# Optimization experiments

Measured on AMD Instinct MI355X. Metric: run time of the kernel, lower is better.

## Reference

```python
import jax, jax.numpy as jnp
import numpy as np

BATCH, SEQ, IN, HID, OUT = 128, 1024, 256, 512, 256


def setup_inputs() -> dict:
    key = jax.random.key(0)
    k_x, k_wi, k_bi, k_wo, k_bo = jax.random.split(key, 5)
    # torch.nn.Linear default init: U(-1/sqrt(fan_in), 1/sqrt(fan_in))
    s_i = 1.0 / np.sqrt(IN + HID)
    s_o = 1.0 / np.sqrt(HID)
    return {
        "x": jax.random.normal(k_x, (BATCH, SEQ, IN), dtype=jnp.float32),
        "W_i2h": jax.random.uniform(k_wi, (HID, IN + HID), jnp.float32, -s_i, s_i),
        "b_i2h": jax.random.uniform(k_bi, (HID,), jnp.float32, -s_i, s_i),
        "W_h2o": jax.random.uniform(k_wo, (OUT, HID), jnp.float32, -s_o, s_o),
        "b_h2o": jax.random.uniform(k_bo, (OUT,), jnp.float32, -s_o, s_o),
    }


def reference(x, W_i2h, b_i2h, W_h2o, b_h2o):
    batch = x.shape[0]
    hid = W_i2h.shape[0]
    # Split i2h weight into input and hidden blocks: cat(x_t, h) @ W.T == x_t @ Wx.T + h @ Wh.T
    Wx = W_i2h[:, : x.shape[-1]]  # (hid, in)
    Wh = W_i2h[:, x.shape[-1] :]  # (hid, hid)
    # Precompute input contributions for all timesteps in one GEMM: (B,S,hid)
    xW = jnp.einsum("bsi,hi->bsh", x, Wx) + b_i2h

    def step(h, xw_t):
        h_new = jnp.tanh(xw_t + h @ Wh.T)
        return h_new, h_new

    h0 = jnp.zeros((batch, hid), dtype=x.dtype)
    h_last, hs = jax.lax.scan(step, h0, jnp.swapaxes(xW, 0, 1))  # hs: (S,B,hid)
    hs = jnp.swapaxes(hs, 0, 1)  # (B,S,hid)
    outputs = jnp.einsum("bsh,oh->bso", hs, W_h2o) + b_h2o  # (B,S,out)
    return outputs, h_last
```

## Files before the change

### kernel.cpp

```cpp
#include <hip/hip_runtime.h>

typedef __attribute__((ext_vector_type(8))) short bf16frag;
typedef __attribute__((ext_vector_type(4))) float f32x4;
typedef __attribute__((ext_vector_type(4))) unsigned int u32x4;

constexpr int B = 128, S = 1024, DI = 256, DH = 512, DO = 256;
constexpr int MAXNB = 16;
constexpr size_t OUT_MAIN = (size_t)B * S * DO;
constexpr size_t SLOT_BYTES = (size_t)B * DH * 2;
constexpr size_t FLAGS_BYTES = 8 * 2 * MAXNB * 64;
constexpr int WH_OFF = 0;
constexpr int WX_OFF = 16384;
constexpr int WHO_OFF = 24576;
constexpr int LDS_BYTES = 65536;

__device__ __forceinline__ void release_vm() {
  asm volatile("s_waitcnt vmcnt(0)" ::: "memory");
}
__device__ __forceinline__ void acquire_cc() {
  asm volatile("" ::: "memory");
}

__device__ __forceinline__ unsigned short f2bf(float f) {
  unsigned int u = __float_as_uint(f);
  u += 0x7fffu + ((u >> 16) & 1u);
  return (unsigned short)(u >> 16);
}
__device__ __forceinline__ float bf2f(unsigned short h) {
  return __uint_as_float(((unsigned int)h) << 16);
}
__device__ __forceinline__ float fast_tanh(float x) {
  float e = __expf(2.0f * x);
  return 1.0f - 2.0f * __builtin_amdgcn_rcpf(e + 1.0f);
}
__device__ __forceinline__ bf16frag cvt8(float4 a, float4 b) {
  bf16frag r;
  r[0]=(short)f2bf(a.x); r[1]=(short)f2bf(a.y); r[2]=(short)f2bf(a.z); r[3]=(short)f2bf(a.w);
  r[4]=(short)f2bf(b.x); r[5]=(short)f2bf(b.y); r[6]=(short)f2bf(b.z); r[7]=(short)f2bf(b.w);
  return r;
}
__device__ __forceinline__ bf16frag load8(const void* base, size_t off, bool fp32m) {
  if (fp32m) {
    const float4* p = reinterpret_cast<const float4*>((const float*)base + off);
    return cvt8(p[0], p[1]);
  }
  return *reinterpret_cast<const bf16frag*>((const unsigned short*)base + off);
}

__device__ __forceinline__ void wait2(const int* a1, int t1, const int* a2, int t2) {
  int guard = 0;
  while (true) {
    int v1 = __hip_atomic_load(a1, __ATOMIC_RELAXED, __HIP_MEMORY_SCOPE_AGENT);
    int v2 = __hip_atomic_load(a2, __ATOMIC_RELAXED, __HIP_MEMORY_SCOPE_AGENT);
    if (v1 >= t1 && v2 >= t2) break;
    if (++guard > (1 << 26)) break;
    __builtin_amdgcn_s_sleep(1);
  }
}

__device__ __forceinline__ void hload16(const unsigned short* hsrc, u32x4* hv) {
  #pragma unroll
  for (int cc = 0; cc < 16; ++cc) {
    const unsigned short* p = hsrc + cc * 32;
    asm volatile("global_load_dwordx4 %0, %1, off sc0 sc1"
                 : "=v"(hv[cc]) : "v"(p) : "memory");
  }
  asm volatile("s_waitcnt vmcnt(0)" ::: "memory");
  __builtin_amdgcn_sched_barrier(0);
}

__global__ void __launch_bounds__(192, 1)
rnn_persistent(const void* __restrict__ xv,
               const void* __restrict__ Wi2hv,
               const void* __restrict__ biv,
               const void* __restrict__ Whov,
               const void* __restrict__ bov,
               void* __restrict__ outv,
               unsigned short* __restrict__ hbuf,
               int* __restrict__ flags,
               int nm, int lg) {
  extern __shared__ unsigned short lds[];
  const int tid = threadIdx.x;
  const int lane = tid & 63;
  const int wave = tid >> 6;
  const int blk = blockIdx.x;
  const int c   = blk & 7;
  const int mem = blk >> 3;
  const int b0  = c * 16;
  const int n_base = mem * 32;
  const int o_base = mem * 16;

  bool fp32m;
  {
    const unsigned short* xu = (const unsigned short*)xv;
    int c0 = 0;
    for (int i = lane; i < 4096; i += 64)
      c0 += (((xu[i] >> 7) & 0xFF) >= 0xC0);
    #pragma unroll
    for (int s = 32; s; s >>= 1) c0 += __shfl_xor(c0, s, 64);
    fp32m = (c0 > 100);
  }

  for (int i = tid; i < 32 * 64; i += 192) {
    int r = i >> 6, bk = i & 63;
    bf16frag v = load8(Wi2hv, (size_t)(n_base + r) * 768 + 256 + bk * 8, fp32m);
    *reinterpret_cast<bf16frag*>(lds + WH_OFF + r * 512 + ((bk ^ (r & 7)) * 8)) = v;
  }
  for (int i = tid; i < 32 * 32; i += 192) {
    int r = i >> 5, bk = i & 31;
    bf16frag v = load8(Wi2hv, (size_t)(n_base + r) * 768 + bk * 8, fp32m);
    *reinterpret_cast<bf16frag*>(lds + WX_OFF + r * 256 + ((bk ^ (r & 7)) * 8)) = v;
  }
  for (int i = tid; i < 16 * 64; i += 192) {
    int r = i >> 6, bk = i & 63;
    bf16frag v = load8(Whov, (size_t)(o_base + r) * 512 + bk * 8, fp32m);
    *reinterpret_cast<bf16frag*>(lds + WHO_OFF + r * 512 + ((bk ^ (r & 7)) * 8)) = v;
  }
  __syncthreads();

  int* cnt = flags + c * (2 * MAXNB * 16);
  const int q  = lane >> 4;
  const int ln = lane & 15;
  float* outf = (float*)outv;
  unsigned short* outh = (unsigned short*)outv;

  if (wave < 2) {
    const int nlB  = wave * 16 + ln;
    const int n_g  = n_base + nlB;
    const float bias = fp32m ? ((const float*)biv)[n_g]
                             : bf2f(((const unsigned short*)biv)[n_g]);
    const int swz = nlB & 7;
    const size_t xrow = (size_t)(b0 + ln) * (S * DI) + q * 8;
    const size_t hrow_off = (size_t)(b0 + ln) * DH + q * 8;

    bf16frag xf[8];
    #pragma unroll
    for (int cc = 0; cc < 8; ++cc)
      xf[cc] = load8(xv, xrow + cc * 32, fp32m);

    for (int t = 0; t < S; ++t) {
      f32x4 acc = {bias, bias, bias, bias};
      #pragma unroll
      for (int cc = 0; cc < 8; ++cc) {
        bf16frag wf = *reinterpret_cast<const bf16frag*>(
            lds + WX_OFF + nlB * 256 + (((cc * 4 + q) ^ swz) * 8));
        acc = __builtin_amdgcn_mfma_f32_16x16x32_bf16(xf[cc], wf, acc, 0, 0, 0);
      }
      if (t + 1 < S) {
        #pragma unroll
        for (int cc = 0; cc < 8; ++cc)
          xf[cc] = load8(xv, xrow + (size_t)(t + 1) * DI + cc * 32, fp32m);
      }
      if (t > 0) {
        const int* a1 = cnt + ((t - 1) & nm) * 16;
        int th1 = 32 * (((t - 1) >> lg) + 1);
        const int* a2 = a1;
        int th2 = th1;
        if (t > nm) { a2 = cnt + (MAXNB + (t & nm)) * 16; th2 = 16 * (t >> lg); }
        wait2(a1, th1, a2, th2);
        acquire_cc();
        const unsigned short* hsrc = hbuf + (size_t)((t - 1) & nm) * (B * DH) + hrow_off;
        u32x4 hv[16];
        hload16(hsrc, hv);
        f32x4 acc2 = {0.f, 0.f, 0.f, 0.f};
        #pragma unroll
        for (int cc = 0; cc < 16; ++cc) {
          union { u32x4 u; bf16frag f; } cv; cv.u = hv[cc];
          bf16frag wf = *reinterpret_cast<const bf16frag*>(
              lds + WH_OFF + nlB * 512 + (((cc * 4 + q) ^ swz) * 8));
          if (cc & 1) acc2 = __builtin_amdgcn_mfma_f32_16x16x32_bf16(cv.f, wf, acc2, 0, 0, 0);
          else        acc  = __builtin_amdgcn_mfma_f32_16x16x32_bf16(cv.f, wf, acc,  0, 0, 0);
        }
        acc += acc2;
      }
      unsigned short* hdst = hbuf + (size_t)(t & nm) * (B * DH);
      #pragma unroll
      for (int r = 0; r < 4; ++r) {
        float hvf = fast_tanh(acc[r]);
        unsigned short hu = f2bf(hvf);
        unsigned int other = __shfl_xor((unsigned int)hu, 1, 64);
        if ((lane & 1) == 0) {
          unsigned int packed = (unsigned int)hu | (other << 16);
          __hip_atomic_store(reinterpret_cast<unsigned int*>(
              hdst + (size_t)(b0 + q * 4 + r) * DH + n_g),
              packed, __ATOMIC_RELAXED, __HIP_MEMORY_SCOPE_AGENT);
        }
        if (t == S - 1) {
          size_t hidx = OUT_MAIN + (size_t)(b0 + q * 4 + r) * DH + n_g;
          if (fp32m) outf[hidx] = hvf; else outh[hidx] = hu;
        }
      }
      release_vm();
      if (lane == 0)
        __hip_atomic_fetch_add(cnt + (t & nm) * 16, 1,
                               __ATOMIC_RELAXED, __HIP_MEMORY_SCOPE_AGENT);
    }
  } else {
    const int o_g = o_base + ln;
    const float bias = fp32m ? ((const float*)bov)[o_g]
                             : bf2f(((const unsigned short*)bov)[o_g]);
    const int swz = ln & 7;
    const size_t hrow_off = (size_t)(b0 + ln) * DH + q * 8;
    for (int u = 0; u < S; ++u) {
      const int* a1 = cnt + (u & nm) * 16;
      int th1 = 32 * ((u >> lg) + 1);
      wait2(a1, th1, a1, th1);
      acquire_cc();
      const unsigned short* hsrc = hbuf + (size_t)(u & nm) * (B * DH) + hrow_off;
      u32x4 hv[16];
      hload16(hsrc, hv);
      if (lane == 0)
        __hip_atomic_fetch_add(cnt + (MAXNB + (u & nm)) * 16, 1,
                               __ATOMIC_RELAXED, __HIP_MEMORY_SCOPE_AGENT);
      f32x4 acc = {bias, bias, bias, bias};
      f32x4 acc2 = {0.f, 0.f, 0.f, 0.f};
      #pragma unroll
      for (int cc = 0; cc < 16; ++cc) {
        union { u32x4 u; bf16frag f; } cv; cv.u = hv[cc];
        bf16frag wf = *reinterpret_cast<const bf16frag*>(
            lds + WHO_OFF + ln * 512 + (((cc * 4 + q) ^ swz) * 8));
        if (cc & 1) acc2 = __builtin_amdgcn_mfma_f32_16x16x32_bf16(cv.f, wf, acc2, 0, 0, 0);
        else        acc  = __builtin_amdgcn_mfma_f32_16x16x32_bf16(cv.f, wf, acc,  0, 0, 0);
      }
      acc += acc2;
      #pragma unroll
      for (int r = 0; r < 4; ++r) {
        size_t oidx = ((size_t)(b0 + q * 4 + r) * S + u) * DO + o_g;
        if (fp32m) outf[oidx] = acc[r]; else outh[oidx] = f2bf(acc[r]);
      }
    }
  }
}

extern "C" void kernel_launch(void* const* d_in, const int* in_sizes, int n_in,
                              void* d_out, int out_size, void* d_ws, size_t ws_size,
                              hipStream_t stream) {
  const void* x    = d_in[0];
  const void* Wi2h = d_in[1];
  const void* bi   = d_in[2];
  const void* Who  = d_in[3];
  const void* bo   = d_in[4];
  void* out = d_out;

  int nb = MAXNB;
  while ((size_t)nb * SLOT_BYTES + FLAGS_BYTES > ws_size && nb > 4) nb >>= 1;
  if ((size_t)nb * SLOT_BYTES + FLAGS_BYTES > ws_size) return;
  int nm = nb - 1;
  int lg = (nb == 16) ? 4 : (nb == 8) ? 3 : 2;

  unsigned short* hbuf = (unsigned short*)d_ws;
  int* flags = (int*)((char*)d_ws + (size_t)nb * SLOT_BYTES);

  hipMemsetAsync(flags, 0, FLAGS_BYTES, stream);

  void* args[] = { (void*)&x, (void*)&Wi2h, (void*)&bi, (void*)&Who, (void*)&bo,
                   (void*)&out, (void*)&hbuf, (void*)&flags, (void*)&nm, (void*)&lg };
  hipError_t e = hipLaunchCooperativeKernel((void*)rnn_persistent, dim3(128), dim3(192),
                                            args, LDS_BYTES, stream);
  if (e != hipSuccess) {
    rnn_persistent<<<dim3(128), dim3(192), LDS_BYTES, stream>>>(
        x, Wi2h, bi, Who, bo, out, hbuf, flags, nm, lg);
  }
}
```

Before: 7.804 ms.

## Tag hidden-state words with step number and share h via LDS ring

Hidden-state entries are now 32-bit words carrying the step tag in the high half, so a consumer can check data readiness directly instead of relying on atomic counter increments. Per-wave flags are written with plain coherent stores and polled across 48 lanes at once. Only wave 0 fetches h from global memory; it packs the values into a 4-slot LDS ring that the second recurrence wave and the output-projection wave read under workgroup-scope flags. This is meant to cut global atomic traffic and duplicate global loads of h on the serial critical path, at the cost of twice the buffer footprint, a larger LDS allocation, and a more intricate handshake with timeout guards.

```diff
diff --git a/kernel.cpp b/kernel.cpp
--- a/kernel.cpp
+++ b/kernel.cpp
@@ -5,21 +5,15 @@
 typedef __attribute__((ext_vector_type(4))) unsigned int u32x4;
 
 constexpr int B = 128, S = 1024, DI = 256, DH = 512, DO = 256;
-constexpr int MAXNB = 16;
 constexpr size_t OUT_MAIN = (size_t)B * S * DO;
-constexpr size_t SLOT_BYTES = (size_t)B * DH * 2;
-constexpr size_t FLAGS_BYTES = 8 * 2 * MAXNB * 64;
+constexpr size_t SLOT_U32 = (size_t)B * DH;
+constexpr size_t SLOT_BYTES = SLOT_U32 * 4;
+constexpr size_t FLAGS_BYTES = 8 * 64 * 4;
 constexpr int WH_OFF = 0;
 constexpr int WX_OFF = 16384;
 constexpr int WHO_OFF = 24576;
-constexpr int LDS_BYTES = 65536;
-
-__device__ __forceinline__ void release_vm() {
-  asm volatile("s_waitcnt vmcnt(0)" ::: "memory");
-}
-__device__ __forceinline__ void acquire_cc() {
-  asm volatile("" ::: "memory");
-}
+constexpr int RING_OFF = 32768;
+constexpr int LDS_BYTES = 131072 + 256;
 
 __device__ __forceinline__ unsigned short f2bf(float f) {
   unsigned int u = __float_as_uint(f);
@@ -47,26 +41,24 @@
   return *reinterpret_cast<const bf16frag*>((const unsigned short*)base + off);
 }
 
-__device__ __forceinline__ void wait2(const int* a1, int t1, const int* a2, int t2) {
-  int guard = 0;
+__device__ __forceinline__ void sc_store(int* p, int v) {
+  asm volatile("global_store_dword %0, %1, off sc0 sc1" :: "v"(p), "v"(v) : "memory");
+}
+
+__device__ __forceinline__ void poll48(const int* cflag, int vthr, int lthr, int skip) {
+  const int lane = threadIdx.x & 63;
+  const int* addr = cflag + (lane < 48 ? lane : 0);
+  int thr = (lane < 32 || lane >= 48) ? vthr : lthr;
+  if (lane == skip) thr = (int)0x80000000;
+  int g = 0;
   while (true) {
-    int v1 = __hip_atomic_load(a1, __ATOMIC_RELAXED, __HIP_MEMORY_SCOPE_AGENT);
-    int v2 = __hip_atomic_load(a2, __ATOMIC_RELAXED, __HIP_MEMORY_SCOPE_AGENT);
-    if (v1 >= t1 && v2 >= t2) break;
-    if (++guard > (1 << 26)) break;
+    int x;
+    asm volatile("global_load_dword %0, %1, off sc0 sc1\n\t"
+                 "s_waitcnt vmcnt(0)" : "=v"(x) : "v"(addr) : "memory");
+    if (__all(x >= thr)) break;
+    if (++g > (1 << 24)) break;
     __builtin_amdgcn_s_sleep(1);
   }
-}
-
-__device__ __forceinline__ void hload16(const unsigned short* hsrc, u32x4* hv) {
-  #pragma unroll
-  for (int cc = 0; cc < 16; ++cc) {
-    const unsigned short* p = hsrc + cc * 32;
-    asm volatile("global_load_dwordx4 %0, %1, off sc0 sc1"
-                 : "=v"(hv[cc]) : "v"(p) : "memory");
-  }
-  asm volatile("s_waitcnt vmcnt(0)" ::: "memory");
-  __builtin_amdgcn_sched_barrier(0);
 }
 
 __global__ void __launch_bounds__(192, 1)
@@ -76,10 +68,12 @@
                const void* __restrict__ Whov,
                const void* __restrict__ bov,
                void* __restrict__ outv,
-               unsigned short* __restrict__ hbuf,
+               unsigned int* __restrict__ hbuf,
                int* __restrict__ flags,
-               int nm, int lg) {
+               int nb) {
   extern __shared__ unsigned short lds[];
+  int* lf  = (int*)((char*)lds + 131072);
+  int* w2p = lf + 1;
   const int tid = threadIdx.x;
   const int lane = tid & 63;
   const int wave = tid >> 6;
@@ -116,29 +110,33 @@
     bf16frag v = load8(Whov, (size_t)(o_base + r) * 512 + bk * 8, fp32m);
     *reinterpret_cast<bf16frag*>(lds + WHO_OFF + r * 512 + ((bk ^ (r & 7)) * 8)) = v;
   }
+  if (tid == 0) { *lf = 0; *w2p = 0; }
   __syncthreads();
 
-  int* cnt = flags + c * (2 * MAXNB * 16);
+  int* cflag = flags + c * 64;
   const int q  = lane >> 4;
   const int ln = lane & 15;
   float* outf = (float*)outv;
   unsigned short* outh = (unsigned short*)outv;
+  char* ringb = (char*)lds + RING_OFF * 2;
 
   if (wave < 2) {
-    const int nlB  = wave * 16 + ln;
-    const int n_g  = n_base + nlB;
+    const int nlB = wave * 16 + ln;
+    const int n_g = n_base + nlB;
     const float bias = fp32m ? ((const float*)biv)[n_g]
                              : bf2f(((const unsigned short*)biv)[n_g]);
     const int swz = nlB & 7;
     const size_t xrow = (size_t)(b0 + ln) * (S * DI) + q * 8;
-    const size_t hrow_off = (size_t)(b0 + ln) * DH + q * 8;
+    const unsigned int* hs_base = hbuf + (size_t)(b0 + ln) * DH + q * 8;
 
     bf16frag xf[8];
     #pragma unroll
     for (int cc = 0; cc < 8; ++cc)
       xf[cc] = load8(xv, xrow + cc * 32, fp32m);
 
-    for (int t = 0; t < S; ++t) {
+    int ps = 0;
+    int pps = 0;
+    for (int v = 0; v < S; ++v) {
       f32x4 acc = {bias, bias, bias, bias};
       #pragma unroll
       for (int cc = 0; cc < 8; ++cc) {
@@ -146,80 +144,159 @@
             lds + WX_OFF + nlB * 256 + (((cc * 4 + q) ^ swz) * 8));
         acc = __builtin_amdgcn_mfma_f32_16x16x32_bf16(xf[cc], wf, acc, 0, 0, 0);
       }
-      if (t + 1 < S) {
+      if (v + 1 < S) {
         #pragma unroll
         for (int cc = 0; cc < 8; ++cc)
-          xf[cc] = load8(xv, xrow + (size_t)(t + 1) * DI + cc * 32, fp32m);
-      }
-      if (t > 0) {
-        const int* a1 = cnt + ((t - 1) & nm) * 16;
-        int th1 = 32 * (((t - 1) >> lg) + 1);
-        const int* a2 = a1;
-        int th2 = th1;
-        if (t > nm) { a2 = cnt + (MAXNB + (t & nm)) * 16; th2 = 16 * (t >> lg); }
-        wait2(a1, th1, a2, th2);
-        acquire_cc();
-        const unsigned short* hsrc = hbuf + (size_t)((t - 1) & nm) * (B * DH) + hrow_off;
-        u32x4 hv[16];
-        hload16(hsrc, hv);
-        f32x4 acc2 = {0.f, 0.f, 0.f, 0.f};
-        #pragma unroll
-        for (int cc = 0; cc < 16; ++cc) {
-          union { u32x4 u; bf16frag f; } cv; cv.u = hv[cc];
-          bf16frag wf = *reinterpret_cast<const bf16frag*>(
-              lds + WH_OFF + nlB * 512 + (((cc * 4 + q) ^ swz) * 8));
-          if (cc & 1) acc2 = __builtin_amdgcn_mfma_f32_16x16x32_bf16(cv.f, wf, acc2, 0, 0, 0);
-          else        acc  = __builtin_amdgcn_mfma_f32_16x16x32_bf16(cv.f, wf, acc,  0, 0, 0);
+          xf[cc] = load8(xv, xrow + (size_t)(v + 1) * DI + cc * 32, fp32m);
+      }
+      if (v > 0) {
+        if (wave == 0) {
+          poll48(cflag, v, v - (nb - 1), 2 * mem);
+          const unsigned int thr = (unsigned int)v << 16;
+          const unsigned int* hs = hs_base + (size_t)pps * SLOT_U32;
+          u32x4 hv[32];
+          int gg = 0;
+          while (true) {
+            #pragma unroll
+            for (int i = 0; i < 32; ++i) {
+              const unsigned int* p = hs + (i >> 1) * 32 + (i & 1) * 4;
+              asm volatile("global_load_dwordx4 %0, %1, off sc0 sc1"
+                           : "=v"(hv[i]) : "v"(p) : "memory");
+            }
+            asm volatile("s_waitcnt vmcnt(0)" ::: "memory");
+            __builtin_amdgcn_sched_barrier(0);
+            bool ok = true;
+            #pragma unroll
+            for (int i = 0; i < 32; ++i) {
+              #pragma unroll
+              for (int e = 0; e < 4; ++e) ok &= (hv[i][e] >= thr);
+            }
+            if (__all(ok)) break;
+            if (++gg > (1 << 16)) break;
+          }
+          if (lane == 0) sc_store(cflag + 32 + mem, v);
+          int g2 = 0;
+          while (__hip_atomic_load(w2p, __ATOMIC_ACQUIRE, __HIP_MEMORY_SCOPE_WORKGROUP)
+                     < v - 4 && ++g2 < (1 << 24))
+            __builtin_amdgcn_s_sleep(1);
+          char* rb = ringb + ((v - 1) & 3) * 16384 + ln * 1024;
+          u32x4 pa[16];
+          #pragma unroll
+          for (int kk = 0; kk < 16; ++kk) {
+            u32x4 t0 = hv[2 * kk], t1 = hv[2 * kk + 1], pk;
+            pk[0] = (t0[0] & 0xFFFFu) | (t0[1] << 16);
+            pk[1] = (t0[2] & 0xFFFFu) | (t0[3] << 16);
+            pk[2] = (t1[0] & 0xFFFFu) | (t1[1] << 16);
+            pk[3] = (t1[2] & 0xFFFFu) | (t1[3] << 16);
+            pa[kk] = pk;
+            int u = kk * 4 + q;
+            *reinterpret_cast<u32x4*>(rb + ((u ^ (ln & 7)) * 16)) = pk;
+          }
+          __hip_atomic_store(lf, v, __ATOMIC_RELEASE, __HIP_MEMORY_SCOPE_WORKGROUP);
+          #pragma unroll
+          for (int kk = 0; kk < 16; ++kk) {
+            union { u32x4 u; bf16frag f; } cv; cv.u = pa[kk];
+            bf16frag wf = *reinterpret_cast<const bf16frag*>(
+                lds + WH_OFF + nlB * 512 + (((kk * 4 + q) ^ swz) * 8));
+            acc = __builtin_amdgcn_mfma_f32_16x16x32_bf16(cv.f, wf, acc, 0, 0, 0);
+          }
+        } else {
+          int g2 = 0;
+          while (__hip_atomic_load(lf, __ATOMIC_ACQUIRE, __HIP_MEMORY_SCOPE_WORKGROUP)
+                     < v && ++g2 < (1 << 24)) {}
+          char* rb = ringb + ((v - 1) & 3) * 16384 + ln * 1024;
+          #pragma unroll
+          for (int kk = 0; kk < 16; ++kk) {
+            int u = kk * 4 + q;
+            u32x4 pk = *reinterpret_cast<const u32x4*>(rb + ((u ^ (ln & 7)) * 16));
+            union { u32x4 u_; bf16frag f; } cv; cv.u_ = pk;
+            bf16frag wf = *reinterpret_cast<const bf16frag*>(
+                lds + WH_OFF + nlB * 512 + (((kk * 4 + q) ^ swz) * 8));
+            acc = __builtin_amdgcn_mfma_f32_16x16x32_bf16(cv.f, wf, acc, 0, 0, 0);
+          }
         }
-        acc += acc2;
-      }
-      unsigned short* hdst = hbuf + (size_t)(t & nm) * (B * DH);
+      }
+      const unsigned int tag = (unsigned int)(v + 1) << 16;
+      unsigned int* hd = hbuf + (size_t)ps * SLOT_U32;
       #pragma unroll
       for (int r = 0; r < 4; ++r) {
         float hvf = fast_tanh(acc[r]);
         unsigned short hu = f2bf(hvf);
-        unsigned int other = __shfl_xor((unsigned int)hu, 1, 64);
-        if ((lane & 1) == 0) {
-          unsigned int packed = (unsigned int)hu | (other << 16);
-          __hip_atomic_store(reinterpret_cast<unsigned int*>(
-              hdst + (size_t)(b0 + q * 4 + r) * DH + n_g),
-              packed, __ATOMIC_RELAXED, __HIP_MEMORY_SCOPE_AGENT);
-        }
-        if (t == S - 1) {
+        unsigned int tw = tag | (unsigned int)hu;
+        unsigned int* p = hd + (size_t)(b0 + q * 4 + r) * DH + n_g;
+        asm volatile("global_store_dword %0, %1, off sc0 sc1"
+                     :: "v"(p), "v"(tw) : "memory");
+        if (v == S - 1) {
           size_t hidx = OUT_MAIN + (size_t)(b0 + q * 4 + r) * DH + n_g;
           if (fp32m) outf[hidx] = hvf; else outh[hidx] = hu;
         }
       }
-      release_vm();
-      if (lane == 0)
-        __hip_atomic_fetch_add(cnt + (t & nm) * 16, 1,
-                               __ATOMIC_RELAXED, __HIP_MEMORY_SCOPE_AGENT);
+      if (lane == 0) sc_store(cflag + 2 * mem + wave, v + 1);
+      pps = ps;
+      ps = (ps + 1 == nb) ? 0 : ps + 1;
+    }
+    if (wave == 0) {
+      poll48(cflag, S, S - (nb - 1), 2 * mem);
+      const unsigned int thr = (unsigned int)S << 16;
+      const unsigned int* hs = hs_base + (size_t)pps * SLOT_U32;
+      u32x4 hv[32];
+      int gg = 0;
+      while (true) {
+        #pragma unroll
+        for (int i = 0; i < 32; ++i) {
+          const unsigned int* p = hs + (i >> 1) * 32 + (i & 1) * 4;
+          asm volatile("global_load_dwordx4 %0, %1, off sc0 sc1"
+                       : "=v"(hv[i]) : "v"(p) : "memory");
+        }
+        asm volatile("s_waitcnt vmcnt(0)" ::: "memory");
+        __builtin_amdgcn_sched_barrier(0);
+        bool ok = true;
+        #pragma unroll
+        for (int i = 0; i < 32; ++i) {
+          #pragma unroll
+          for (int e = 0; e < 4; ++e) ok &= (hv[i][e] >= thr);
+        }
+        if (__all(ok)) break;
+        if (++gg > (1 << 16)) break;
+      }
+      int g2 = 0;
+      while (__hip_atomic_load(w2p, __ATOMIC_ACQUIRE, __HIP_MEMORY_SCOPE_WORKGROUP)
+                 < S - 4 && ++g2 < (1 << 24))
+        __builtin_amdgcn_s_sleep(1);
+      char* rb = ringb + ((S - 1) & 3) * 16384 + ln * 1024;
+      #pragma unroll
+      for (int kk = 0; kk < 16; ++kk) {
+        u32x4 t0 = hv[2 * kk], t1 = hv[2 * kk + 1], pk;
+        pk[0] = (t0[0] & 0xFFFFu) | (t0[1] << 16);
+        pk[1] = (t0[2] & 0xFFFFu) | (t0[3] << 16);
+        pk[2] = (t1[0] & 0xFFFFu) | (t1[1] << 16);
+        pk[3] = (t1[2] & 0xFFFFu) | (t1[3] << 16);
+        int u = kk * 4 + q;
+        *reinterpret_cast<u32x4*>(rb + ((u ^ (ln & 7)) * 16)) = pk;
+      }
+      __hip_atomic_store(lf, S, __ATOMIC_RELEASE, __HIP_MEMORY_SCOPE_WORKGROUP);
     }
   } else {
     const int o_g = o_base + ln;
     const float bias = fp32m ? ((const float*)bov)[o_g]
                              : bf2f(((const unsigned short*)bov)[o_g]);
-    const int swz = ln & 7;
-    const size_t hrow_off = (size_t)(b0 + ln) * DH + q * 8;
+    const int swzW = ln & 7;
     for (int u = 0; u < S; ++u) {
-      const int* a1 = cnt + (u & nm) * 16;
-      int th1 = 32 * ((u >> lg) + 1);
-      wait2(a1, th1, a1, th1);
-      acquire_cc();
-      const unsigned short* hsrc = hbuf + (size_t)(u & nm) * (B * DH) + hrow_off;
-      u32x4 hv[16];
-      hload16(hsrc, hv);
-      if (lane == 0)
-        __hip_atomic_fetch_add(cnt + (MAXNB + (u & nm)) * 16, 1,
-                               __ATOMIC_RELAXED, __HIP_MEMORY_SCOPE_AGENT);
+      int g2 = 0;
+      while (__hip_atomic_load(lf, __ATOMIC_ACQUIRE, __HIP_MEMORY_SCOPE_WORKGROUP)
+                 < u + 1 && ++g2 < (1 << 24))
+        __builtin_amdgcn_s_sleep(1);
+      char* rb = ringb + (u & 3) * 16384 + ln * 1024;
       f32x4 acc = {bias, bias, bias, bias};
       f32x4 acc2 = {0.f, 0.f, 0.f, 0.f};
       #pragma unroll
-      for (int cc = 0; cc < 16; ++cc) {
-        union { u32x4 u; bf16frag f; } cv; cv.u = hv[cc];
+      for (int kk = 0; kk < 16; ++kk) {
+        int uu = kk * 4 + q;
+        u32x4 pk = *reinterpret_cast<const u32x4*>(rb + ((uu ^ (ln & 7)) * 16));
+        union { u32x4 a; bf16frag f; } cv; cv.a = pk;
         bf16frag wf = *reinterpret_cast<const bf16frag*>(
-            lds + WHO_OFF + ln * 512 + (((cc * 4 + q) ^ swz) * 8));
-        if (cc & 1) acc2 = __builtin_amdgcn_mfma_f32_16x16x32_bf16(cv.f, wf, acc2, 0, 0, 0);
+            lds + WHO_OFF + ln * 512 + (((kk * 4 + q) ^ swzW) * 8));
+        if (kk & 1) acc2 = __builtin_amdgcn_mfma_f32_16x16x32_bf16(cv.f, wf, acc2, 0, 0, 0);
         else        acc  = __builtin_amdgcn_mfma_f32_16x16x32_bf16(cv.f, wf, acc,  0, 0, 0);
       }
       acc += acc2;
@@ -228,6 +305,7 @@
         size_t oidx = ((size_t)(b0 + q * 4 + r) * S + u) * DO + o_g;
         if (fp32m) outf[oidx] = acc[r]; else outh[oidx] = f2bf(acc[r]);
       }
+      __hip_atomic_store(w2p, u + 1, __ATOMIC_RELEASE, __HIP_MEMORY_SCOPE_WORKGROUP);
     }
   }
 }
@@ -242,23 +320,28 @@
   const void* bo   = d_in[4];
   void* out = d_out;
 
-  int nb = MAXNB;
-  while ((size_t)nb * SLOT_BYTES + FLAGS_BYTES > ws_size && nb > 4) nb >>= 1;
+  int nb = 4;
+  while ((size_t)nb * SLOT_BYTES + FLAGS_BYTES > ws_size && nb > 2) nb--;
   if ((size_t)nb * SLOT_BYTES + FLAGS_BYTES > ws_size) return;
-  int nm = nb - 1;
-  int lg = (nb == 16) ? 4 : (nb == 8) ? 3 : 2;
-
-  unsigned short* hbuf = (unsigned short*)d_ws;
+
+  unsigned int* hbuf = (unsigned int*)d_ws;
   int* flags = (int*)((char*)d_ws + (size_t)nb * SLOT_BYTES);
 
-  hipMemsetAsync(flags, 0, FLAGS_BYTES, stream);
+  hipMemsetAsync(d_ws, 0, (size_t)nb * SLOT_BYTES + FLAGS_BYTES, stream);
+
+  static int attr_done = 0;
+  if (!attr_done) {
+    hipFuncSetAttribute((const void*)rnn_persistent,
+                        hipFuncAttributeMaxDynamicSharedMemorySize, LDS_BYTES);
+    attr_done = 1;
+  }
 
   void* args[] = { (void*)&x, (void*)&Wi2h, (void*)&bi, (void*)&Who, (void*)&bo,
-                   (void*)&out, (void*)&hbuf, (void*)&flags, (void*)&nm, (void*)&lg };
+                   (void*)&out, (void*)&hbuf, (void*)&flags, (void*)&nb };
   hipError_t e = hipLaunchCooperativeKernel((void*)rnn_persistent, dim3(128), dim3(192),
                                             args, LDS_BYTES, stream);
   if (e != hipSuccess) {
     rnn_persistent<<<dim3(128), dim3(192), LDS_BYTES, stream>>>(
-        x, Wi2h, bi, Who, bo, out, hbuf, flags, nm, lg);
-  }
-}
+        x, Wi2h, bi, Who, bo, out, hbuf, flags, nb);
+  }
+}
```

After: 8.211 ms. 5.2% more time.
